# Kernel optimization log

Hardware: AMD Instinct MI355X
Metric: run time of the kernel (lower is better)

Reference implementation:

```python
import jax, jax.numpy as jnp
import numpy as np

EPS = 1e-5  # BatchNorm1d eps


def _glorot(key, shape):
    fan_in, fan_out = shape[0], shape[1]
    lim = float(np.sqrt(6.0 / (fan_in + fan_out)))
    return jax.random.uniform(key, shape, jnp.float32, -lim, lim)


def setup_inputs() -> dict:
    key = jax.random.key(0)
    ks = jax.random.split(key, 6)
    N, IN, H, OUT = 50000, 128, 64, 64
    E = 800000
    x = jax.random.normal(ks[0], (N, IN), jnp.float32)
    edge_index = jax.random.randint(ks[1], (2, E), 0, N, jnp.int64)
    return {
        "x": x,
        "edge_index": edge_index,
        "W1": _glorot(ks[2], (IN, H)),
        "b1": jnp.zeros((H,), jnp.float32),
        "gamma1": jnp.ones((H,), jnp.float32),
        "beta1": jnp.zeros((H,), jnp.float32),
        "W2": _glorot(ks[3], (H, OUT)),
        "b2": jnp.zeros((OUT,), jnp.float32),
        "gamma2": jnp.ones((OUT,), jnp.float32),
        "beta2": jnp.zeros((OUT,), jnp.float32),
    }


def _gcn_conv(x, W, b, src, dst, norm, n):
    # x' = D^{-1/2} (A + I) D^{-1/2} X W + b  (PyG GCNConv, edge_weight=None)
    h = x @ W                              # [N, F]
    msg = h[src] * norm[:, None]           # gather + scale, [E+N, F]
    out = jax.ops.segment_sum(msg, dst, num_segments=n)  # scatter-add
    return out + b


def _batch_norm(h, gamma, beta):
    # training-mode BN over node dim, biased variance (as torch uses for normalization)
    mean = h.mean(0)
    var = h.var(0)
    return (h - mean) * jax.lax.rsqrt(var + EPS) * gamma + beta


def reference(x, edge_index, W1, b1, gamma1, beta1, W2, b2, gamma2, beta2):
    n = x.shape[0]
    # add self loops
    loop = jnp.arange(n, dtype=edge_index.dtype)
    src = jnp.concatenate([edge_index[0], loop])
    dst = jnp.concatenate([edge_index[1], loop])
    # symmetric degree normalization (deg >= 1 thanks to self loops)
    deg = jax.ops.segment_sum(jnp.ones(src.shape[0], x.dtype), dst, num_segments=n)
    dinv = jax.lax.rsqrt(jnp.maximum(deg, 1e-12))
    norm = dinv[src] * dinv[dst]           # [E+N]

    # layer 1: GCNConv -> BN -> ReLU (dropout = identity in eval)
    h = _gcn_conv(x, W1, b1, src, dst, norm, n)
    h = jax.nn.relu(_batch_norm(h, gamma1, beta1))
    # layer 2: GCNConv -> BN (no activation on last layer)
    h = _gcn_conv(h, W2, b2, src, dst, norm, n)
    h = _batch_norm(h, gamma2, beta2)
    return h
```

## Files before the change

### kernel.cpp

```cpp
#include <hip/hip_runtime.h>
#include <hip/hip_fp16.h>
#include <math.h>

#define EPS 1e-5f
#define CAP 64

typedef float v4f __attribute__((ext_vector_type(4)));

__device__ __forceinline__ float xor32sum(float a) {
    return a + __shfl_xor(a, 32, 64);
}

__global__ void k_init(int* __restrict__ cnt, float* __restrict__ stats,
                       __half* __restrict__ Ylo, __half* __restrict__ Yhi,
                       unsigned short* __restrict__ csr, int N) {
    int i = blockIdx.x * blockDim.x + threadIdx.x;
    if (i < N) {
        cnt[i] = 0;
        int4* p = (int4*)(csr + (size_t)i * CAP);
#pragma unroll
        for (int k = 0; k < 8; ++k) p[k] = make_int4(-1, -1, -1, -1);
    }
    if (i < 256) stats[i] = 0.0f;
    if (i < 16) {
        ((int*)(Ylo + (size_t)N * 32))[i] = 0;
        ((int*)(Yhi + (size_t)N * 32))[i] = 0;
    }
}

__global__ __launch_bounds__(256) void k_gemm1_fill(const float* __restrict__ x,
                                                    const float* __restrict__ W1,
                                                    __half* __restrict__ Ylo,
                                                    __half* __restrict__ Yhi, int N,
                                                    const int* __restrict__ src,
                                                    const int* __restrict__ dst,
                                                    int* __restrict__ cnt,
                                                    unsigned short* __restrict__ csr,
                                                    int E, int G) {
    if ((int)blockIdx.x >= G) {
        int t = (blockIdx.x - G) * 256 + threadIdx.x;
        int stride = (gridDim.x - G) * 256;
        for (int e = t; e < E; e += stride) {
            int d = dst[e];
            int pos = atomicAdd(&cnt[d], 1);
            if (pos < CAP)
                __builtin_nontemporal_store((unsigned short)src[e], &csr[(size_t)d * CAP + pos]);
        }
        return;
    }
    __shared__ float w[128 * 64];
    for (int i = threadIdx.x; i < 128 * 64; i += 256) w[i] = W1[i];
    __syncthreads();
    int lane = threadIdx.x & 63;
    int wave = threadIdx.x >> 6;
    int half = lane >> 5, l = lane & 31;
    __half* Yout = half ? Yhi : Ylo;
    int gwave = blockIdx.x * 4 + wave;
    int nw = G * 4;
    for (int r0 = gwave * 4; r0 < N; r0 += nw * 4) {
        int nr = min(4, N - r0);
        const float4* x0 = (const float4*)(x + (size_t)__builtin_amdgcn_readfirstlane(r0) * 128);
        const float4* x1 = (const float4*)(x + (size_t)__builtin_amdgcn_readfirstlane(min(r0 + 1, N - 1)) * 128);
        const float4* x2 = (const float4*)(x + (size_t)__builtin_amdgcn_readfirstlane(min(r0 + 2, N - 1)) * 128);
        const float4* x3 = (const float4*)(x + (size_t)__builtin_amdgcn_readfirstlane(min(r0 + 3, N - 1)) * 128);
        float a0 = 0.f, a1 = 0.f, a2 = 0.f, a3 = 0.f;
#pragma unroll 4
        for (int kc = 0; kc < 32; ++kc) {
            float4 v0 = x0[kc], v1 = x1[kc], v2 = x2[kc], v3 = x3[kc];
            const float* wp = &w[kc * 256 + lane];
            float wk0 = wp[0], wk1 = wp[64], wk2 = wp[128], wk3 = wp[192];
            a0 += v0.x * wk0 + v0.y * wk1 + v0.z * wk2 + v0.w * wk3;
            a1 += v1.x * wk0 + v1.y * wk1 + v1.z * wk2 + v1.w * wk3;
            a2 += v2.x * wk0 + v2.y * wk1 + v2.z * wk2 + v2.w * wk3;
            a3 += v3.x * wk0 + v3.y * wk1 + v3.z * wk2 + v3.w * wk3;
        }
        Yout[(size_t)(r0 + 0) * 32 + l] = __float2half(a0);
        if (nr > 1) Yout[(size_t)(r0 + 1) * 32 + l] = __float2half(a1);
        if (nr > 2) Yout[(size_t)(r0 + 2) * 32 + l] = __float2half(a2);
        if (nr > 3) Yout[(size_t)(r0 + 3) * 32 + l] = __float2half(a3);
    }
}

__global__ void k_scale(const int* __restrict__ cnt, float* __restrict__ dinv,
                        __half* __restrict__ Ylo, __half* __restrict__ Yhi, int N) {
    int i = blockIdx.x * blockDim.x + threadIdx.x;
    if (i == 0) dinv[N] = 0.0f;
    int row = i >> 2, c4 = i & 3;
    if (row >= N) return;
    float dv = rsqrtf((float)(cnt[row] + 1));
    if (c4 == 0) dinv[row] = dv;
    union U16 { uint4 u; __half2 h[4]; } t;
#pragma unroll
    for (int buf = 0; buf < 2; ++buf) {
        __half* Y = buf ? Yhi : Ylo;
        uint4* p = (uint4*)(Y + (size_t)row * 32 + c4 * 8);
        t.u = *p;
#pragma unroll
        for (int k = 0; k < 4; ++k) {
            float2 f = __half22float2(t.h[k]);
            t.h[k] = __float22half2_rn(make_float2(f.x * dv, f.y * dv));
        }
        *p = t.u;
    }
}

__global__ __launch_bounds__(256) void k_agg(const __half* __restrict__ Ylo,
                                             const __half* __restrict__ Yhi,
                                             const unsigned short* __restrict__ csr,
                                             const int* __restrict__ cnt,
                                             const float* __restrict__ dinv,
                                             float* __restrict__ H,
                                             float* __restrict__ stats, int N) {
    __shared__ float ssum[4][32], ssq[4][32];
    int half = blockIdx.x & 1;
    const __half* Y = half ? Yhi : Ylo;
    int lane = threadIdx.x & 63;
    int wave = threadIdx.x >> 6;
    int fl = lane & 3;
    int node = (lane >> 2) & 3;
    int g = lane >> 4;
    int gd = g >> 1;
    int gsh = (g & 1) << 4;
    float selfmask = (g == 0) ? 1.f : 0.f;
    int slot = (blockIdx.x >> 1) * 4 + wave;
    int nslots = (gridDim.x >> 1) * 4;
    float s[8], q[8];
#pragma unroll
    for (int j = 0; j < 8; ++j) { s[j] = 0.f; q[j] = 0.f; }
    union U16 { uint4 u; __half2 h[4]; };
    for (int base = slot * 4; base < N; base += nslots * 4) {
        int myv = base + node;
        bool vok = myv < N;
        int vs = vok ? myv : N;
        int c  = vok ? min(cnt[myv], CAP) : 0;
        float dv = dinv[vs];
        const unsigned int* crow =
            (const unsigned int*)(csr + (size_t)(vok ? myv : 0) * CAP);
        float a[8];
        {
            U16 t; t.u = *(const uint4*)(Y + (size_t)vs * 32 + fl * 8);
#pragma unroll
            for (int k = 0; k < 4; ++k) {
                float2 f = __half22float2(t.h[k]);
                a[2 * k]     = selfmask * f.x;
                a[2 * k + 1] = selfmask * f.y;
            }
        }
        for (int b = 0; b < 16; ++b) {
            if (__all(4 * b >= c)) break;
            unsigned int w = crow[2 * b + gd];
            int ent = vok ? (int)((w >> gsh) & 0xFFFFu) : 0xFFFF;
            int idx = min(ent, N);
            U16 t; t.u = *(const uint4*)(Y + (size_t)idx * 32 + fl * 8);
#pragma unroll
            for (int k = 0; k < 4; ++k) {
                float2 f = __half22float2(t.h[k]);
                a[2 * k]     += f.x;
                a[2 * k + 1] += f.y;
            }
        }
#pragma unroll
        for (int j = 0; j < 8; ++j) {
            a[j] += __shfl_xor(a[j], 16, 64);
            a[j] = xor32sum(a[j]) * dv;
        }
        if (g == 0 && vok) {
            v4f lo = {a[0], a[1], a[2], a[3]};
            v4f hi = {a[4], a[5], a[6], a[7]};
            float* dst = H + (size_t)myv * 64 + half * 32 + fl * 8;
            __builtin_nontemporal_store(lo, (v4f*)dst);
            __builtin_nontemporal_store(hi, (v4f*)(dst + 4));
        }
#pragma unroll
        for (int j = 0; j < 8; ++j) { s[j] += a[j]; q[j] += a[j] * a[j]; }
    }
#pragma unroll
    for (int j = 0; j < 8; ++j) {
        s[j] += __shfl_xor(s[j], 4, 64); s[j] += __shfl_xor(s[j], 8, 64);
        q[j] += __shfl_xor(q[j], 4, 64); q[j] += __shfl_xor(q[j], 8, 64);
    }
    if (lane < 4) {
#pragma unroll
        for (int j = 0; j < 8; ++j) {
            ssum[wave][fl * 8 + j] = s[j];
            ssq[wave][fl * 8 + j]  = q[j];
        }
    }
    __syncthreads();
    if (threadIdx.x < 32) {
        float ts = ssum[0][threadIdx.x] + ssum[1][threadIdx.x] + ssum[2][threadIdx.x] + ssum[3][threadIdx.x];
        float tq = ssq[0][threadIdx.x] + ssq[1][threadIdx.x] + ssq[2][threadIdx.x] + ssq[3][threadIdx.x];
        atomicAdd(&stats[half * 32 + threadIdx.x], ts);
        atomicAdd(&stats[64 + half * 32 + threadIdx.x], tq);
    }
}

__global__ __launch_bounds__(256) void k_gemm2(const float* __restrict__ H1,
                                               const float* __restrict__ stats,
                                               const float* __restrict__ gamma,
                                               const float* __restrict__ beta,
                                               const float* __restrict__ W2,
                                               const float* __restrict__ dinv,
                                               __half* __restrict__ Ylo,
                                               __half* __restrict__ Yhi, int N) {
    __shared__ float w[64 * 64];
    __shared__ float xs[4][64][4];
    for (int i = threadIdx.x; i < 64 * 64; i += 256) w[i] = W2[i];
    int lane = threadIdx.x & 63;
    int wave = threadIdx.x >> 6;
    int half = lane >> 5, l = lane & 31;
    __half* Yout = half ? Yhi : Ylo;
    float mean = stats[lane] / (float)N;
    float var = stats[64 + lane] / (float)N - mean * mean;
    float rstd = rsqrtf(var + EPS);
    float scale = rstd * gamma[lane];
    float shift = beta[lane] - mean * scale;
    __syncthreads();
    int gwave = blockIdx.x * 4 + wave;
    int nw = gridDim.x * 4;
    for (int r0 = gwave * 4; r0 < N; r0 += nw * 4) {
        int nr = min(4, N - r0);
#pragma unroll
        for (int j = 0; j < 4; ++j) {
            float v = 0.f;
            if (j < nr) {
                v = H1[(size_t)(r0 + j) * 64 + lane];
                v = fmaxf(v * scale + shift, 0.f);
            }
            xs[wave][lane][j] = v;
        }
        float a0 = 0.f, a1 = 0.f, a2 = 0.f, a3 = 0.f;
#pragma unroll 8
        for (int k = 0; k < 64; ++k) {
            float wk = w[k * 64 + lane];
            float4 xv = *(const float4*)&xs[wave][k][0];
            a0 += xv.x * wk; a1 += xv.y * wk; a2 += xv.z * wk; a3 += xv.w * wk;
        }
        Yout[(size_t)(r0 + 0) * 32 + l] = __float2half(a0 * dinv[r0]);
        if (nr > 1) Yout[(size_t)(r0 + 1) * 32 + l] = __float2half(a1 * dinv[r0 + 1]);
        if (nr > 2) Yout[(size_t)(r0 + 2) * 32 + l] = __float2half(a2 * dinv[r0 + 2]);
        if (nr > 3) Yout[(size_t)(r0 + 3) * 32 + l] = __float2half(a3 * dinv[r0 + 3]);
    }
}

__global__ void k_bnfinal(float* __restrict__ out, const float* __restrict__ stats,
                          const float* __restrict__ gamma, const float* __restrict__ beta,
                          int N) {
    int i = blockIdx.x * blockDim.x + threadIdx.x;
    int total = N * 64;
    if (i < total) {
        int f = i & 63;
        float mean = stats[f] / (float)N;
        float var = stats[64 + f] / (float)N - mean * mean;
        float rstd = rsqrtf(var + EPS);
        out[i] = (out[i] - mean) * rstd * gamma[f] + beta[f];
    }
}

extern "C" void kernel_launch(void* const* d_in, const int* in_sizes, int n_in,
                              void* d_out, int out_size, void* d_ws, size_t ws_size,
                              hipStream_t stream) {
    const float* x      = (const float*)d_in[0];
    const int*   ei     = (const int*)d_in[1];
    const float* W1     = (const float*)d_in[2];
    const float* gamma1 = (const float*)d_in[4];
    const float* beta1  = (const float*)d_in[5];
    const float* W2     = (const float*)d_in[6];
    const float* gamma2 = (const float*)d_in[8];
    const float* beta2  = (const float*)d_in[9];
    float* out = (float*)d_out;

    const int N = in_sizes[0] / 128;
    const int E = in_sizes[1] / 2;
    const int* src = ei;
    const int* dst = ei + E;

    char* ws = (char*)d_ws;
    int*   cnt   = (int*)  ws;
    float* stats = (float*)(ws + 0x40000);
    float* dinv  = (float*)(ws + 0x50000);
    __half* Ylo  = (__half*)(ws + 0x90000);
    __half* Yhi  = (__half*)(ws + 0x90000 + 0x320000);
    float* H1    = (float*)(ws + 0x90000 + 0x640000);
    unsigned short* csr = (unsigned short*)(ws + 0x90000 + 0x640000 + 0xC40000);

    const int B = (N + 255) / 256;
    const int total = N * 64;
    const int G = 512, F = 768;

    k_init<<<B, 256, 0, stream>>>(cnt, stats, Ylo, Yhi, csr, N);

    k_gemm1_fill<<<G + F, 256, 0, stream>>>(x, W1, Ylo, Yhi, N, src, dst, cnt, csr, E, G);
    k_scale<<<(N * 4 + 255) / 256, 256, 0, stream>>>(cnt, dinv, Ylo, Yhi, N);
    k_agg<<<1250, 256, 0, stream>>>(Ylo, Yhi, csr, cnt, dinv, H1, stats, N);

    k_gemm2<<<1024, 256, 0, stream>>>(H1, stats, gamma1, beta1, W2, dinv, Ylo, Yhi, N);
    k_agg<<<1250, 256, 0, stream>>>(Ylo, Yhi, csr, cnt, dinv, out, stats + 128, N);
    k_bnfinal<<<(total + 255) / 256, 256, 0, stream>>>(out, stats + 128, gamma2, beta2, N);
}
```

Baseline: 273.5 us.

## Stage x rows in LDS for 8-row GEMM1 tiles and rebalance fill/GEMM blocks

The GEMM1 part now copies 8 rows of x per wave into shared memory with coalesced float2 loads, then computes 8 output rows per weight fetch instead of 4 rows read straight from global memory. This doubles reuse of each W1 value loaded from LDS and replaces scalar-addressed global loads with coalesced ones. The fill blocks now come first in the grid and the block split changes from 512 GEMM and 768 fill to 768 GEMM and 256 fill. There is no barrier between the per-wave LDS writes and reads, which relies on wave-level execution order, and the extra 16KB of LDS per block may lower occupancy.

```diff
diff --git a/kernel.cpp b/kernel.cpp
--- a/kernel.cpp
+++ b/kernel.cpp
@@ -36,10 +36,10 @@
                                                     const int* __restrict__ dst,
                                                     int* __restrict__ cnt,
                                                     unsigned short* __restrict__ csr,
-                                                    int E, int G) {
-    if ((int)blockIdx.x >= G) {
-        int t = (blockIdx.x - G) * 256 + threadIdx.x;
-        int stride = (gridDim.x - G) * 256;
+                                                    int E, int F, int G) {
+    if ((int)blockIdx.x < F) {
+        int t = blockIdx.x * 256 + threadIdx.x;
+        int stride = F * 256;
         for (int e = t; e < E; e += stride) {
             int d = dst[e];
             int pos = atomicAdd(&cnt[d], 1);
@@ -49,35 +49,36 @@
         return;
     }
     __shared__ float w[128 * 64];
+    __shared__ float xs[4][8][128];
     for (int i = threadIdx.x; i < 128 * 64; i += 256) w[i] = W1[i];
     __syncthreads();
     int lane = threadIdx.x & 63;
     int wave = threadIdx.x >> 6;
     int half = lane >> 5, l = lane & 31;
     __half* Yout = half ? Yhi : Ylo;
-    int gwave = blockIdx.x * 4 + wave;
+    int gwave = (blockIdx.x - F) * 4 + wave;
     int nw = G * 4;
-    for (int r0 = gwave * 4; r0 < N; r0 += nw * 4) {
-        int nr = min(4, N - r0);
-        const float4* x0 = (const float4*)(x + (size_t)__builtin_amdgcn_readfirstlane(r0) * 128);
-        const float4* x1 = (const float4*)(x + (size_t)__builtin_amdgcn_readfirstlane(min(r0 + 1, N - 1)) * 128);
-        const float4* x2 = (const float4*)(x + (size_t)__builtin_amdgcn_readfirstlane(min(r0 + 2, N - 1)) * 128);
-        const float4* x3 = (const float4*)(x + (size_t)__builtin_amdgcn_readfirstlane(min(r0 + 3, N - 1)) * 128);
-        float a0 = 0.f, a1 = 0.f, a2 = 0.f, a3 = 0.f;
+    for (int r0 = gwave * 8; r0 < N; r0 += nw * 8) {
+        int nr = min(8, N - r0);
+        for (int j = 0; j < nr; ++j)
+            *(float2*)&xs[wave][j][lane * 2] =
+                *(const float2*)(x + (size_t)(r0 + j) * 128 + lane * 2);
+        float acc[8];
+#pragma unroll
+        for (int j = 0; j < 8; ++j) acc[j] = 0.f;
 #pragma unroll 4
         for (int kc = 0; kc < 32; ++kc) {
-            float4 v0 = x0[kc], v1 = x1[kc], v2 = x2[kc], v3 = x3[kc];
             const float* wp = &w[kc * 256 + lane];
             float wk0 = wp[0], wk1 = wp[64], wk2 = wp[128], wk3 = wp[192];
-            a0 += v0.x * wk0 + v0.y * wk1 + v0.z * wk2 + v0.w * wk3;
-            a1 += v1.x * wk0 + v1.y * wk1 + v1.z * wk2 + v1.w * wk3;
-            a2 += v2.x * wk0 + v2.y * wk1 + v2.z * wk2 + v2.w * wk3;
-            a3 += v3.x * wk0 + v3.y * wk1 + v3.z * wk2 + v3.w * wk3;
-        }
-        Yout[(size_t)(r0 + 0) * 32 + l] = __float2half(a0);
-        if (nr > 1) Yout[(size_t)(r0 + 1) * 32 + l] = __float2half(a1);
-        if (nr > 2) Yout[(size_t)(r0 + 2) * 32 + l] = __float2half(a2);
-        if (nr > 3) Yout[(size_t)(r0 + 3) * 32 + l] = __float2half(a3);
+#pragma unroll
+            for (int j = 0; j < 8; ++j) {
+                float4 xv = *(const float4*)&xs[wave][j][kc * 4];
+                acc[j] += xv.x * wk0 + xv.y * wk1 + xv.z * wk2 + xv.w * wk3;
+            }
+        }
+#pragma unroll
+        for (int j = 0; j < 8; ++j)
+            if (j < nr) Yout[(size_t)(r0 + j) * 32 + l] = __float2half(acc[j]);
     }
 }
 
@@ -286,11 +287,11 @@
 
     const int B = (N + 255) / 256;
     const int total = N * 64;
-    const int G = 512, F = 768;
+    const int G = 768, F = 256;
 
     k_init<<<B, 256, 0, stream>>>(cnt, stats, Ylo, Yhi, csr, N);
 
-    k_gemm1_fill<<<G + F, 256, 0, stream>>>(x, W1, Ylo, Yhi, N, src, dst, cnt, csr, E, G);
+    k_gemm1_fill<<<F + G, 256, 0, stream>>>(x, W1, Ylo, Yhi, N, src, dst, cnt, csr, E, F, G);
     k_scale<<<(N * 4 + 255) / 256, 256, 0, stream>>>(cnt, dinv, Ylo, Yhi, N);
     k_agg<<<1250, 256, 0, stream>>>(Ylo, Yhi, csr, cnt, dinv, H1, stats, N);
 
```

New measurement: 267.3 us. -2.3%, faster.
